# Optimization experiments

Hardware: AMD Instinct MI355X
Metric: run time of the kernel (lower is better)

The kernel has to match this reference:

```python
import jax, jax.numpy as jnp
import numpy as np

H = 8  # LSTM units for both layers


def lstm_forward(x, W, U, b, return_sequences):
    """Keras-style LSTM. x: [B,T,F], W: [F,4H], U: [H,4H], b: [4H]. Gate order i,f,g,o."""
    B = x.shape[0]
    h_dim = U.shape[0]
    # precompute input projection for all timesteps: [T,B,4H]
    xz = jnp.swapaxes(jnp.einsum('btf,fg->btg', x, W) + b, 0, 1)

    def step(carry, zt):
        h, c = carry
        z = zt + h @ U
        i, f, g, o = jnp.split(z, 4, axis=-1)
        c = jax.nn.sigmoid(f) * c + jax.nn.sigmoid(i) * jnp.tanh(g)
        h = jax.nn.sigmoid(o) * jnp.tanh(c)
        return (h, c), h

    h0 = jnp.zeros((B, h_dim), x.dtype)
    (hT, _), hs = jax.lax.scan(step, (h0, h0), xz)
    return jnp.swapaxes(hs, 0, 1) if return_sequences else hT


def setup_inputs() -> dict:
    key = jax.random.key(0)
    ks = jax.random.split(key, 16)
    B, T, F, FUT = 8192, 256, 16, 8
    s = 0.1
    return {
        'img': jax.random.normal(ks[0], (B, 1), jnp.float32),
        'past_metadata': jax.random.normal(ks[1], (B, T, F), jnp.float32),
        'future_metadata': jax.random.normal(ks[2], (B, FUT), jnp.float32),
        'W1': jax.random.normal(ks[3], (F, 4 * H), jnp.float32) * s,
        'U1': jax.random.normal(ks[4], (H, 4 * H), jnp.float32) * s,
        'b1': jnp.zeros((4 * H,), jnp.float32),
        'W2': jax.random.normal(ks[5], (H, 4 * H), jnp.float32) * s,
        'U2': jax.random.normal(ks[6], (H, 4 * H), jnp.float32) * s,
        'b2': jnp.zeros((4 * H,), jnp.float32),
        'Wd1': jax.random.normal(ks[7], (H + FUT, 8), jnp.float32) * s,
        'bd1': jnp.zeros((8,), jnp.float32),
        'Wd2': jax.random.normal(ks[8], (8, 8), jnp.float32) * s,
        'bd2': jnp.zeros((8,), jnp.float32),
        'Wo': jax.random.normal(ks[9], (8, 4), jnp.float32) * s,
        'bo': jnp.zeros((4,), jnp.float32),
    }


def reference(img, past_metadata, future_metadata, W1, U1, b1, W2, U2, b2,
              Wd1, bd1, Wd2, bd2, Wo, bo):
    # img is accepted but unused, matching the original call().
    x = lstm_forward(past_metadata, W1, U1, b1, return_sequences=True)   # [B,T,H]
    x = lstm_forward(x, W2, U2, b2, return_sequences=False)             # [B,H]
    x = jnp.concatenate([x, future_metadata], axis=1)                    # [B,H+FUT]
    x = jax.nn.relu(x @ Wd1 + bd1)
    x = jax.nn.relu(x @ Wd2 + bd2)
    return x @ Wo + bo                                                   # [B,4]
```

## Files before the change

### kernel.cpp

```cpp
#include <hip/hip_runtime.h>

#define T_STEPS 256
#define LPB     16
#define BLOCK   256
#define B_PER_BLOCK (BLOCK / LPB)

#define PIN(v) asm volatile("" : "+v"(v))

#define ROR1 0x121
#define ROR8 0x128

template<int CTRL>
__device__ __forceinline__ float dppf(float x) {
    return __int_as_float(__builtin_amdgcn_update_dpp(
        0, __float_as_int(x), CTRL, 0xF, 0xF, true));
}

__device__ __forceinline__ float fsig(float x) {
    return __builtin_amdgcn_rcpf(1.0f + __builtin_amdgcn_exp2f(-1.44269504088896f * x));
}
__device__ __forceinline__ float ftanh(float x) {
    return fmaf(__builtin_amdgcn_rcpf(1.0f + __builtin_amdgcn_exp2f(-2.88539008177793f * x)),
                2.0f, -1.0f);
}
__device__ __forceinline__ float fsig_or_tanh(float z, float sc, float off) {
    float r = __builtin_amdgcn_rcpf(1.0f + __builtin_amdgcn_exp2f(-1.44269504088896f * sc * z));
    return fmaf(r, sc, off);
}

__attribute__((amdgpu_waves_per_eu(2, 2)))
__global__ __launch_bounds__(BLOCK)
void lstm_dpp_kernel(const float* __restrict__ past,
                     const float* __restrict__ fut,
                     const float* __restrict__ W1,
                     const float* __restrict__ U1,
                     const float* __restrict__ b1,
                     const float* __restrict__ W2,
                     const float* __restrict__ U2,
                     const float* __restrict__ b2,
                     const float* __restrict__ Wd1,
                     const float* __restrict__ bd1,
                     const float* __restrict__ Wd2,
                     const float* __restrict__ bd2,
                     const float* __restrict__ Wo,
                     const float* __restrict__ bo,
                     float* __restrict__ out)
{
    const int tid = threadIdx.x;
    const int l   = tid & (LPB - 1);
    const int j   = l & 7;
    const int r   = l >> 3;
    const int b   = blockIdx.x * B_PER_BLOCK + (tid >> 4);
    const int colA = l, colB = 16 + l;

    float wA[16], wB[16];
#pragma unroll
    for (int f = 0; f < 16; ++f) { wA[f] = W1[f * 32 + colA]; wB[f] = W1[f * 32 + colB]; }
    float uAr[8], uBr[8], w2Ar[8], w2Br[8], u2Ar[8], u2Br[8];
#pragma unroll
    for (int rr = 0; rr < 8; ++rr) {
        const int k = (j - rr) & 7;
        uAr[rr]  = U1[k * 32 + colA];  uBr[rr]  = U1[k * 32 + colB];
        w2Ar[rr] = W2[k * 32 + colA];  w2Br[rr] = W2[k * 32 + colB];
        u2Ar[rr] = U2[k * 32 + colA];  u2Br[rr] = U2[k * 32 + colB];
    }
    float bA = b1[colA], bB = b1[colB], b2A = b2[colA], b2B = b2[colB];

    PIN(bA); PIN(bB); PIN(b2A); PIN(b2B);
#pragma unroll
    for (int f = 0; f < 16; ++f) { PIN(wA[f]); PIN(wB[f]); }
#pragma unroll
    for (int rr = 0; rr < 8; ++rr) {
        PIN(uAr[rr]); PIN(uBr[rr]); PIN(w2Ar[rr]); PIN(w2Br[rr]); PIN(u2Ar[rr]); PIN(u2Br[rr]);
    }

    const float sc  = r ? 1.0f :  2.0f;
    const float off = r ? 0.0f : -1.0f;
    const float* xrow = past + (size_t)b * (T_STEPS * 16);

    float c1 = 0.f, c2 = 0.f, h1d = 0.f, h2d = 0.f;

#define XT(xv, idx) zA##_c0 = fmaf(xv, wA[idx], zA##_c0); zB##_c0 = fmaf(xv, wB[idx], zB##_c0)
#define XU(xv, idx) zA##_c1 = fmaf(xv, wA[idx], zA##_c1); zB##_c1 = fmaf(xv, wB[idx], zB##_c1)

    auto step = [&](float4 q0, float4 q1, float4 q2, float4 q3) {
        float zA_c0 = bA, zB_c0 = bB, zA_c1 = 0.f, zB_c1 = 0.f;
        XT(q0.x, 0);  XU(q0.y, 1);  XT(q0.z, 2);  XU(q0.w, 3);
        XT(q1.x, 4);  XU(q1.y, 5);  XT(q1.z, 6);  XU(q1.w, 7);
        XT(q2.x, 8);  XU(q2.y, 9);  XT(q2.z, 10); XU(q2.w, 11);
        XT(q3.x, 12); XU(q3.y, 13); XT(q3.z, 14); XU(q3.w, 15);
        float hr = h1d;
        zA_c0 = fmaf(hr, uAr[0], zA_c0); zB_c0 = fmaf(hr, uBr[0], zB_c0);
#pragma unroll
        for (int rr = 1; rr < 8; ++rr) {
            hr = dppf<ROR1>(hr);
            if (rr & 1) { zA_c1 = fmaf(hr, uAr[rr], zA_c1); zB_c1 = fmaf(hr, uBr[rr], zB_c1); }
            else        { zA_c0 = fmaf(hr, uAr[rr], zA_c0); zB_c0 = fmaf(hr, uBr[rr], zB_c0); }
        }
        const float zA = zA_c0 + zA_c1, zB = zB_c0 + zB_c1;

        float sA = fsig(zA);
        float vB = fsig_or_tanh(zB, sc, off);
        float p  = sA * vB;
        float e1 = dppf<ROR8>(r ? sA : p);
        float e2 = dppf<ROR8>(vB);
        float fh = r ? sA : e1;
        float pp = r ? e1 : p;
        float oh = r ? vB : e2;
        c1  = fmaf(fh, c1, pp);
        h1d = oh * ftanh(c1);

        float g1 = h1d, g2 = h2d;
        float yA_c0 = b2A, yB_c0 = b2B, yA_c1 = 0.f, yB_c1 = 0.f;
        yA_c0 = fmaf(g1, w2Ar[0], yA_c0); yB_c0 = fmaf(g1, w2Br[0], yB_c0);
        yA_c1 = fmaf(g2, u2Ar[0], yA_c1); yB_c1 = fmaf(g2, u2Br[0], yB_c1);
#pragma unroll
        for (int rr = 1; rr < 8; ++rr) {
            g1 = dppf<ROR1>(g1);
            g2 = dppf<ROR1>(g2);
            if (rr & 1) {
                yA_c1 = fmaf(g1, w2Ar[rr], yA_c1); yB_c1 = fmaf(g1, w2Br[rr], yB_c1);
                yA_c0 = fmaf(g2, u2Ar[rr], yA_c0); yB_c0 = fmaf(g2, u2Br[rr], yB_c0);
            } else {
                yA_c0 = fmaf(g1, w2Ar[rr], yA_c0); yB_c0 = fmaf(g1, w2Br[rr], yB_c0);
                yA_c1 = fmaf(g2, u2Ar[rr], yA_c1); yB_c1 = fmaf(g2, u2Br[rr], yB_c1);
            }
        }
        const float zA2 = yA_c0 + yA_c1, zB2 = yB_c0 + yB_c1;

        float sA2 = fsig(zA2);
        float vB2 = fsig_or_tanh(zB2, sc, off);
        float p2  = sA2 * vB2;
        float f1  = dppf<ROR8>(r ? sA2 : p2);
        float f2  = dppf<ROR8>(vB2);
        float fh2 = r ? sA2 : f1;
        float pp2 = r ? f1  : p2;
        float oh2 = r ? vB2 : f2;
        c2  = fmaf(fh2, c2, pp2);
        h2d = oh2 * ftanh(c2);
    };
#undef XT
#undef XU

    float4 A0 = *(const float4*)(xrow + 0),  A1 = *(const float4*)(xrow + 4);
    float4 A2 = *(const float4*)(xrow + 8),  A3 = *(const float4*)(xrow + 12);
    float4 B0 = *(const float4*)(xrow + 16), B1 = *(const float4*)(xrow + 20);
    float4 B2 = *(const float4*)(xrow + 24), B3 = *(const float4*)(xrow + 28);

    for (int t = 0; t < T_STEPS; t += 2) {
        step(A0, A1, A2, A3);
        {
            const int ta = (t + 2 < T_STEPS) ? t + 2 : 0;
            const float* pa = xrow + ta * 16;
            A0 = *(const float4*)(pa + 0); A1 = *(const float4*)(pa + 4);
            A2 = *(const float4*)(pa + 8); A3 = *(const float4*)(pa + 12);
        }
        step(B0, B1, B2, B3);
        {
            const int tb = (t + 3 < T_STEPS) ? t + 3 : 0;
            const float* pb = xrow + tb * 16;
            B0 = *(const float4*)(pb + 0); B1 = *(const float4*)(pb + 4);
            B2 = *(const float4*)(pb + 8); B3 = *(const float4*)(pb + 12);
        }
    }

    float fm[8];
#pragma unroll
    for (int k = 0; k < 8; ++k) fm[k] = fut[b * 8 + k];

    float s1 = bd1[j];
    {
        float t2 = h2d;
        s1 = fmaf(t2, Wd1[j * 8 + j], s1);
#pragma unroll
        for (int rr = 1; rr < 8; ++rr) {
            t2 = dppf<ROR1>(t2);
            s1 = fmaf(t2, Wd1[((j - rr) & 7) * 8 + j], s1);
        }
    }
#pragma unroll
    for (int k = 0; k < 8; ++k) s1 = fmaf(fm[k], Wd1[(8 + k) * 8 + j], s1);
    s1 = fmaxf(s1, 0.f);

    float s2 = bd2[j];
    {
        float t3 = s1;
        s2 = fmaf(t3, Wd2[j * 8 + j], s2);
#pragma unroll
        for (int rr = 1; rr < 8; ++rr) {
            t3 = dppf<ROR1>(t3);
            s2 = fmaf(t3, Wd2[((j - rr) & 7) * 8 + j], s2);
        }
    }
    s2 = fmaxf(s2, 0.f);

    float d2a[8];
    {
        float t4 = s2;
        d2a[0] = t4;
#pragma unroll
        for (int rr = 1; rr < 8; ++rr) { t4 = dppf<ROR1>(t4); d2a[rr] = t4; }
    }
    if (l < 4) {
        float so = bo[l];
#pragma unroll
        for (int rr = 0; rr < 8; ++rr) so = fmaf(d2a[rr], Wo[((l - rr) & 7) * 4 + l], so);
        out[b * 4 + l] = so;
    }
}

extern "C" void kernel_launch(void* const* d_in, const int* in_sizes, int n_in,
                              void* d_out, int out_size, void* d_ws, size_t ws_size,
                              hipStream_t stream) {
    const float* past = (const float*)d_in[1];
    const float* fut  = (const float*)d_in[2];
    const float* W1   = (const float*)d_in[3];
    const float* U1   = (const float*)d_in[4];
    const float* b1   = (const float*)d_in[5];
    const float* W2   = (const float*)d_in[6];
    const float* U2   = (const float*)d_in[7];
    const float* b2   = (const float*)d_in[8];
    const float* Wd1  = (const float*)d_in[9];
    const float* bd1  = (const float*)d_in[10];
    const float* Wd2  = (const float*)d_in[11];
    const float* bd2  = (const float*)d_in[12];
    const float* Wo   = (const float*)d_in[13];
    const float* bo   = (const float*)d_in[14];
    float* out = (float*)d_out;

    const int B = in_sizes[2] / 8;
    const int grid = (B * LPB) / BLOCK;

    lstm_dpp_kernel<<<grid, BLOCK, 0, stream>>>(
        past, fut, W1, U1, b1, W2, U2, b2,
        Wd1, bd1, Wd2, bd2, Wo, bo, out);
}
```

Measured before the change: 337.7 us.

## Stream inputs through an LDS ring via global_load_lds and use packed FMA

Each wave now streams its input rows into a per-wave shared-memory ring buffer of four slots, using asynchronous global_load_lds with a vmcnt wait, instead of holding float4 prefetches in registers. Each slot covers four timesteps. The gate matmuls are rewritten on two-wide float vectors so the compiler can emit packed FMA instructions, and the rotated h1 values are cached in packed form for the next step. The goals are to halve the FMA issue count, cut register pressure, and hide global-load latency. The cost is an extra horizontal add per gate, LDS reads on every step, and a reliance on raw waitcnt ordering being correct without barriers.

```diff
diff --git a/kernel.cpp b/kernel.cpp
--- a/kernel.cpp
+++ b/kernel.cpp
@@ -4,8 +4,12 @@
 #define LPB     16
 #define BLOCK   256
 #define B_PER_BLOCK (BLOCK / LPB)
-
-#define PIN(v) asm volatile("" : "+v"(v))
+#define WAVES   (BLOCK / 64)
+#define NSLOT   4
+
+typedef float v2f __attribute__((ext_vector_type(2)));
+
+#define PIN2(v) asm volatile("" : "+v"(v))
 
 #define ROR1 0x121
 #define ROR8 0x128
@@ -30,139 +34,141 @@
 
 __attribute__((amdgpu_waves_per_eu(2, 2)))
 __global__ __launch_bounds__(BLOCK)
-void lstm_dpp_kernel(const float* __restrict__ past,
-                     const float* __restrict__ fut,
-                     const float* __restrict__ W1,
-                     const float* __restrict__ U1,
-                     const float* __restrict__ b1,
-                     const float* __restrict__ W2,
-                     const float* __restrict__ U2,
-                     const float* __restrict__ b2,
-                     const float* __restrict__ Wd1,
-                     const float* __restrict__ bd1,
-                     const float* __restrict__ Wd2,
-                     const float* __restrict__ bd2,
-                     const float* __restrict__ Wo,
-                     const float* __restrict__ bo,
-                     float* __restrict__ out)
+void lstm_pk_kernel(const float* __restrict__ past,
+                    const float* __restrict__ fut,
+                    const float* __restrict__ W1,
+                    const float* __restrict__ U1,
+                    const float* __restrict__ b1,
+                    const float* __restrict__ W2,
+                    const float* __restrict__ U2,
+                    const float* __restrict__ b2,
+                    const float* __restrict__ Wd1,
+                    const float* __restrict__ bd1,
+                    const float* __restrict__ Wd2,
+                    const float* __restrict__ bd2,
+                    const float* __restrict__ Wo,
+                    const float* __restrict__ bo,
+                    float* __restrict__ out)
 {
     const int tid = threadIdx.x;
     const int l   = tid & (LPB - 1);
     const int j   = l & 7;
     const int r   = l >> 3;
-    const int b   = blockIdx.x * B_PER_BLOCK + (tid >> 4);
+    const int g   = tid >> 4;
+    const int gw  = g & 3;
+    const int wid = tid >> 6;
+    const int b   = blockIdx.x * B_PER_BLOCK + g;
     const int colA = l, colB = 16 + l;
 
-    float wA[16], wB[16];
-#pragma unroll
-    for (int f = 0; f < 16; ++f) { wA[f] = W1[f * 32 + colA]; wB[f] = W1[f * 32 + colB]; }
-    float uAr[8], uBr[8], w2Ar[8], w2Br[8], u2Ar[8], u2Br[8];
-#pragma unroll
-    for (int rr = 0; rr < 8; ++rr) {
-        const int k = (j - rr) & 7;
-        uAr[rr]  = U1[k * 32 + colA];  uBr[rr]  = U1[k * 32 + colB];
-        w2Ar[rr] = W2[k * 32 + colA];  w2Br[rr] = W2[k * 32 + colB];
-        u2Ar[rr] = U2[k * 32 + colA];  u2Br[rr] = U2[k * 32 + colB];
+    __shared__ float ring[WAVES][NSLOT][256];
+
+    v2f wAp[8], wBp[8];
+#pragma unroll
+    for (int c = 0; c < 8; ++c) {
+        wAp[c] = v2f{W1[(2*c)*32 + colA], W1[(2*c+1)*32 + colA]};
+        wBp[c] = v2f{W1[(2*c)*32 + colB], W1[(2*c+1)*32 + colB]};
+    }
+    v2f uAp[4], uBp[4], w2Ap[4], w2Bp[4], u2Ap[4], u2Bp[4];
+#pragma unroll
+    for (int c = 0; c < 4; ++c) {
+        const int k0 = (j - 2*c) & 7, k1 = (j - (2*c+1)) & 7;
+        uAp[c]  = v2f{U1[k0*32 + colA], U1[k1*32 + colA]};
+        uBp[c]  = v2f{U1[k0*32 + colB], U1[k1*32 + colB]};
+        w2Ap[c] = v2f{W2[k0*32 + colA], W2[k1*32 + colA]};
+        w2Bp[c] = v2f{W2[k0*32 + colB], W2[k1*32 + colB]};
+        u2Ap[c] = v2f{U2[k0*32 + colA], U2[k1*32 + colA]};
+        u2Bp[c] = v2f{U2[k0*32 + colB], U2[k1*32 + colB]};
     }
     float bA = b1[colA], bB = b1[colB], b2A = b2[colA], b2B = b2[colB];
 
-    PIN(bA); PIN(bB); PIN(b2A); PIN(b2B);
-#pragma unroll
-    for (int f = 0; f < 16; ++f) { PIN(wA[f]); PIN(wB[f]); }
-#pragma unroll
-    for (int rr = 0; rr < 8; ++rr) {
-        PIN(uAr[rr]); PIN(uBr[rr]); PIN(w2Ar[rr]); PIN(w2Br[rr]); PIN(u2Ar[rr]); PIN(u2Br[rr]);
+#pragma unroll
+    for (int c = 0; c < 8; ++c) { PIN2(wAp[c]); PIN2(wBp[c]); }
+#pragma unroll
+    for (int c = 0; c < 4; ++c) {
+        PIN2(uAp[c]); PIN2(uBp[c]); PIN2(w2Ap[c]); PIN2(w2Bp[c]); PIN2(u2Ap[c]); PIN2(u2Bp[c]);
     }
 
     const float sc  = r ? 1.0f :  2.0f;
     const float off = r ? 0.0f : -1.0f;
-    const float* xrow = past + (size_t)b * (T_STEPS * 16);
+
+    const float* srcbase = past + (size_t)b * (T_STEPS * 16) + (l >> 2) * 16 + (l & 3) * 4;
+
+#pragma unroll
+    for (int s = 0; s < NSLOT; ++s)
+        __builtin_amdgcn_global_load_lds(srcbase + s * 64, &ring[wid][s][0], 16, 0, 0);
 
     float c1 = 0.f, c2 = 0.f, h1d = 0.f, h2d = 0.f;
-
-#define XT(xv, idx) zA##_c0 = fmaf(xv, wA[idx], zA##_c0); zB##_c0 = fmaf(xv, wB[idx], zB##_c0)
-#define XU(xv, idx) zA##_c1 = fmaf(xv, wA[idx], zA##_c1); zB##_c1 = fmaf(xv, wB[idx], zB##_c1)
-
-    auto step = [&](float4 q0, float4 q1, float4 q2, float4 q3) {
-        float zA_c0 = bA, zB_c0 = bB, zA_c1 = 0.f, zB_c1 = 0.f;
-        XT(q0.x, 0);  XU(q0.y, 1);  XT(q0.z, 2);  XU(q0.w, 3);
-        XT(q1.x, 4);  XU(q1.y, 5);  XT(q1.z, 6);  XU(q1.w, 7);
-        XT(q2.x, 8);  XU(q2.y, 9);  XT(q2.z, 10); XU(q2.w, 11);
-        XT(q3.x, 12); XU(q3.y, 13); XT(q3.z, 14); XU(q3.w, 15);
-        float hr = h1d;
-        zA_c0 = fmaf(hr, uAr[0], zA_c0); zB_c0 = fmaf(hr, uBr[0], zB_c0);
-#pragma unroll
-        for (int rr = 1; rr < 8; ++rr) {
-            hr = dppf<ROR1>(hr);
-            if (rr & 1) { zA_c1 = fmaf(hr, uAr[rr], zA_c1); zB_c1 = fmaf(hr, uBr[rr], zB_c1); }
-            else        { zA_c0 = fmaf(hr, uAr[rr], zA_c0); zB_c0 = fmaf(hr, uBr[rr], zB_c0); }
+    v2f h1r2[4];
+#pragma unroll
+    for (int c = 0; c < 4; ++c) h1r2[c] = v2f{0.f, 0.f};
+
+    for (int t = 0; t < T_STEPS; t += 4) {
+        const int slot = (t >> 2) & (NSLOT - 1);
+        asm volatile("s_waitcnt vmcnt(3)" ::: "memory");
+        __builtin_amdgcn_sched_barrier(0);
+        const v2f* sx = (const v2f*)&ring[wid][slot][gw * 64];
+
+#pragma unroll
+        for (int q = 0; q < 4; ++q) {
+            const v2f* xp = sx + q * 8;
+
+            v2f aA = v2f{bA, 0.f}, aB = v2f{bB, 0.f};
+#pragma unroll
+            for (int c = 0; c < 8; ++c) {
+                const v2f xv = xp[c];
+                aA = xv * wAp[c] + aA;
+                aB = xv * wBp[c] + aB;
+            }
+#pragma unroll
+            for (int c = 0; c < 4; ++c) {
+                aA = h1r2[c] * uAp[c] + aA;
+                aB = h1r2[c] * uBp[c] + aB;
+            }
+            const float zA = aA.x + aA.y, zB = aB.x + aB.y;
+
+            float sA = fsig(zA);
+            float vB = fsig_or_tanh(zB, sc, off);
+            float p  = sA * vB;
+            float e1 = dppf<ROR8>(r ? sA : p);
+            float e2 = dppf<ROR8>(vB);
+            float fh = r ? sA : e1;
+            float pp = r ? e1 : p;
+            float oh = r ? vB : e2;
+            c1  = fmaf(fh, c1, pp);
+            h1d = oh * ftanh(c1);
+
+            v2f dA = v2f{b2A, 0.f}, dB = v2f{b2B, 0.f};
+            float g1v = h1d, g2v = h2d;
+#pragma unroll
+            for (int c = 0; c < 4; ++c) {
+                v2f G1, G2;
+                G1.x = g1v;  G2.x = g2v;
+                g1v = dppf<ROR1>(g1v);  g2v = dppf<ROR1>(g2v);
+                G1.y = g1v;  G2.y = g2v;
+                if (c < 3) { g1v = dppf<ROR1>(g1v); g2v = dppf<ROR1>(g2v); }
+                h1r2[c] = G1;
+                dA = G1 * w2Ap[c] + dA;  dB = G1 * w2Bp[c] + dB;
+                dA = G2 * u2Ap[c] + dA;  dB = G2 * u2Bp[c] + dB;
+            }
+            const float zA2 = dA.x + dA.y, zB2 = dB.x + dB.y;
+
+            float sA2 = fsig(zA2);
+            float vB2 = fsig_or_tanh(zB2, sc, off);
+            float p2  = sA2 * vB2;
+            float f1  = dppf<ROR8>(r ? sA2 : p2);
+            float f2  = dppf<ROR8>(vB2);
+            float fh2 = r ? sA2 : f1;
+            float pp2 = r ? f1  : p2;
+            float oh2 = r ? vB2 : f2;
+            c2  = fmaf(fh2, c2, pp2);
+            h2d = oh2 * ftanh(c2);
         }
-        const float zA = zA_c0 + zA_c1, zB = zB_c0 + zB_c1;
-
-        float sA = fsig(zA);
-        float vB = fsig_or_tanh(zB, sc, off);
-        float p  = sA * vB;
-        float e1 = dppf<ROR8>(r ? sA : p);
-        float e2 = dppf<ROR8>(vB);
-        float fh = r ? sA : e1;
-        float pp = r ? e1 : p;
-        float oh = r ? vB : e2;
-        c1  = fmaf(fh, c1, pp);
-        h1d = oh * ftanh(c1);
-
-        float g1 = h1d, g2 = h2d;
-        float yA_c0 = b2A, yB_c0 = b2B, yA_c1 = 0.f, yB_c1 = 0.f;
-        yA_c0 = fmaf(g1, w2Ar[0], yA_c0); yB_c0 = fmaf(g1, w2Br[0], yB_c0);
-        yA_c1 = fmaf(g2, u2Ar[0], yA_c1); yB_c1 = fmaf(g2, u2Br[0], yB_c1);
-#pragma unroll
-        for (int rr = 1; rr < 8; ++rr) {
-            g1 = dppf<ROR1>(g1);
-            g2 = dppf<ROR1>(g2);
-            if (rr & 1) {
-                yA_c1 = fmaf(g1, w2Ar[rr], yA_c1); yB_c1 = fmaf(g1, w2Br[rr], yB_c1);
-                yA_c0 = fmaf(g2, u2Ar[rr], yA_c0); yB_c0 = fmaf(g2, u2Br[rr], yB_c0);
-            } else {
-                yA_c0 = fmaf(g1, w2Ar[rr], yA_c0); yB_c0 = fmaf(g1, w2Br[rr], yB_c0);
-                yA_c1 = fmaf(g2, u2Ar[rr], yA_c1); yB_c1 = fmaf(g2, u2Br[rr], yB_c1);
-            }
-        }
-        const float zA2 = yA_c0 + yA_c1, zB2 = yB_c0 + yB_c1;
-
-        float sA2 = fsig(zA2);
-        float vB2 = fsig_or_tanh(zB2, sc, off);
-        float p2  = sA2 * vB2;
-        float f1  = dppf<ROR8>(r ? sA2 : p2);
-        float f2  = dppf<ROR8>(vB2);
-        float fh2 = r ? sA2 : f1;
-        float pp2 = r ? f1  : p2;
-        float oh2 = r ? vB2 : f2;
-        c2  = fmaf(fh2, c2, pp2);
-        h2d = oh2 * ftanh(c2);
-    };
-#undef XT
-#undef XU
-
-    float4 A0 = *(const float4*)(xrow + 0),  A1 = *(const float4*)(xrow + 4);
-    float4 A2 = *(const float4*)(xrow + 8),  A3 = *(const float4*)(xrow + 12);
-    float4 B0 = *(const float4*)(xrow + 16), B1 = *(const float4*)(xrow + 20);
-    float4 B2 = *(const float4*)(xrow + 24), B3 = *(const float4*)(xrow + 28);
-
-    for (int t = 0; t < T_STEPS; t += 2) {
-        step(A0, A1, A2, A3);
-        {
-            const int ta = (t + 2 < T_STEPS) ? t + 2 : 0;
-            const float* pa = xrow + ta * 16;
-            A0 = *(const float4*)(pa + 0); A1 = *(const float4*)(pa + 4);
-            A2 = *(const float4*)(pa + 8); A3 = *(const float4*)(pa + 12);
-        }
-        step(B0, B1, B2, B3);
-        {
-            const int tb = (t + 3 < T_STEPS) ? t + 3 : 0;
-            const float* pb = xrow + tb * 16;
-            B0 = *(const float4*)(pb + 0); B1 = *(const float4*)(pb + 4);
-            B2 = *(const float4*)(pb + 8); B3 = *(const float4*)(pb + 12);
-        }
-    }
+
+        const int tnext = t + NSLOT * 4;
+        const float* rs = (tnext < T_STEPS) ? (srcbase + tnext * 16) : srcbase;
+        __builtin_amdgcn_global_load_lds(rs, &ring[wid][slot][0], 16, 0, 0);
+    }
+    asm volatile("s_waitcnt vmcnt(0)" ::: "memory");
 
     float fm[8];
 #pragma unroll
@@ -231,7 +237,7 @@
     const int B = in_sizes[2] / 8;
     const int grid = (B * LPB) / BLOCK;
 
-    lstm_dpp_kernel<<<grid, BLOCK, 0, stream>>>(
+    lstm_pk_kernel<<<grid, BLOCK, 0, stream>>>(
         past, fut, W1, U1, b1, W2, U2, b2,
         Wd1, bd1, Wd2, bd2, Wo, bo, out);
 }
```

Result: faster. 289.6 us (-14.2%).
